# Kernel tuning notes

Hardware: AMD Instinct MI355X
Metric: run time of the kernel (lower is better)

## Reference

```python
import jax, jax.numpy as jnp
import numpy as np

N_NODES = 100000
N_EDGES = 1600000
D_FEAT = 64


def setup_inputs() -> dict:
    key = jax.random.key(0)
    k1, k2 = jax.random.split(key)
    x = jax.random.normal(k1, (N_NODES, D_FEAT), dtype=jnp.float32)
    edge_index = jax.random.randint(k2, (2, N_EDGES), 0, N_NODES, dtype=jnp.int64)
    return {"x": x, "edge_index": edge_index}


def reference(x, edge_index):
    # GCNProp (improved=False): remove self loops, add self loops w/ weight 1,
    # symmetric deg^-1/2 normalization, then spmm aggregation.
    N = x.shape[0]
    row, col = edge_index[0], edge_index[1]
    # remove_self_loops: zero the weight of any self-loop edge (math-equivalent
    # to dropping it, and jit-friendly: no data-dependent shapes).
    w = jnp.where(row != col, jnp.ones((), x.dtype), jnp.zeros((), x.dtype))
    # add_self_loops: append N diagonal edges with loop_value = 1 (improved=False)
    loop = jnp.arange(N, dtype=row.dtype)
    row_a = jnp.concatenate([row, loop])          # [E+N]
    col_a = jnp.concatenate([col, loop])          # [E+N]
    w_a = jnp.concatenate([w, jnp.ones((N,), x.dtype)])  # [E+N]
    # degree via scatter_add over rows
    deg = jax.ops.segment_sum(w_a, row_a, num_segments=N)  # [N]
    # deg^-0.5 with inf -> 0
    dinv = jnp.where(deg > 0, jax.lax.rsqrt(deg), jnp.zeros((), x.dtype))
    # edge normalization: deg[row]^-1/2 * w * deg[col]^-1/2
    norm = dinv[row_a] * w_a * dinv[col_a]        # [E+N]
    # spmm: gather neighbor features, scale, scatter-add into rows
    out = jax.ops.segment_sum(norm[:, None] * x[col_a], row_a, num_segments=N)  # [N, D]
    return out
```

## Files before the change

### kernel.cpp

```cpp
#include <hip/hip_runtime.h>

#define N_NODES 100000
#define N_EDGES 1600000
#define D 64
#define NB 391
#define BCAP 4480
#define PBLK 256
#define TPB 512
#define CHUNK ((N_EDGES + PBLK - 1) / PBLK)
#define CURSTRIDE 32

__device__ __forceinline__ unsigned short f2b(float f) {
    unsigned u = __float_as_uint(f);
    u += 0x7FFF + ((u >> 16) & 1);
    return (unsigned short)(u >> 16);
}
__device__ __forceinline__ float b2f(unsigned short v) {
    return __uint_as_float(((unsigned)v) << 16);
}

__global__ void init_cursor_kernel(int* __restrict__ cursor) {
    int b = blockIdx.x * blockDim.x + threadIdx.x;
    if (b < NB) cursor[b * CURSTRIDE] = b * BCAP;
}

__global__ void scatter_direct_kernel(const int* __restrict__ ei, int* __restrict__ cursor,
                                      int* __restrict__ epack) {
    __shared__ int h[NB];
    __shared__ int lbase[NB];
    __shared__ int lcur[NB];
    int t = threadIdx.x;
    for (int i = t; i < NB; i += TPB) h[i] = 0;
    __syncthreads();
    int s = blockIdx.x * CHUNK;
    int e = min(s + CHUNK, N_EDGES);
    for (int i = s + t; i < e; i += TPB) {
        int r = ei[i], c = ei[N_EDGES + i];
        if (r != c) atomicAdd(&h[r >> 8], 1);
    }
    __syncthreads();
    for (int i = t; i < NB; i += TPB) {
        lbase[i] = atomicAdd(&cursor[i * CURSTRIDE], h[i]);
        lcur[i] = 0;
    }
    __syncthreads();
    for (int i = s + t; i < e; i += TPB) {
        int r = ei[i], c = ei[N_EDGES + i];
        if (r != c) {
            int b = r >> 8;
            int p = lbase[b] + atomicAdd(&lcur[b], 1);
            epack[p] = ((r & 255) << 17) | c;
        }
    }
}

__global__ void rowsort_convert_kernel(const int* __restrict__ cursor, int* __restrict__ epack,
                                       int* __restrict__ rowstart, int* __restrict__ rowend,
                                       float* __restrict__ dinv, const float* __restrict__ x,
                                       unsigned short* __restrict__ xs) {
    __shared__ int ebuf[BCAP];
    __shared__ int h[256];
    __shared__ int sc[256];
    __shared__ int cur[256];
    __shared__ float dv[256];
    int b = blockIdx.x;
    int t = threadIdx.x;
    int base = b * BCAP;
    int n = min(cursor[b * CURSTRIDE] - base, BCAP);
    for (int i = t; i < n; i += 256) ebuf[i] = epack[base + i];
    h[t] = 0;
    __syncthreads();
    for (int i = t; i < n; i += 256) atomicAdd(&h[ebuf[i] >> 17], 1);
    __syncthreads();
    int v = h[t];
    sc[t] = v;
    __syncthreads();
    for (int off = 1; off < 256; off <<= 1) {
        int u = (t >= off) ? sc[t - off] : 0;
        __syncthreads();
        sc[t] += u;
        __syncthreads();
    }
    int excl = sc[t] - v;
    int row = b * 256 + t;
    float di = rsqrtf((float)(1 + v));
    if (row < N_NODES) {
        rowstart[row] = base + excl;
        rowend[row] = base + excl + v;
        dinv[row] = di;
    }
    dv[t] = di;
    cur[t] = excl;
    __syncthreads();
    for (int i = t; i < n; i += 256) {
        int p = ebuf[i];
        int pos = atomicAdd(&cur[p >> 17], 1);
        epack[base + pos] = p & 0x1FFFF;
    }
    int nrows = min(256, N_NODES - b * 256);
    const float4* x4 = (const float4*)x;
    ushort4* xs4 = (ushort4*)xs;
    for (int i = t; i < nrows * 16; i += 256) {
        int rl = i >> 4;
        float4 vv = x4[(size_t)(b * 256 + rl) * 16 + (i & 15)];
        float dd = dv[rl];
        ushort4 o;
        o.x = f2b(vv.x * dd);
        o.y = f2b(vv.y * dd);
        o.z = f2b(vv.z * dd);
        o.w = f2b(vv.w * dd);
        xs4[(size_t)(b * 256 + rl) * 16 + (i & 15)] = o;
    }
}

__global__ void gather_kernel(const unsigned short* __restrict__ xs, const float* __restrict__ dinv,
                              const int* __restrict__ rowstart, const int* __restrict__ rowend,
                              const int* __restrict__ sortedCol, float* __restrict__ out) {
    int t = blockIdx.x * blockDim.x + threadIdx.x;
    int r = t >> 6;
    int d = t & 63;
    if (r >= N_NODES) return;
    int start = rowstart[r];
    int end = rowend[r];
    float dr = dinv[r];
    float acc = b2f(xs[r * D + d]);
    for (int j = start; j < end; j += 64) {
        int idx = j + d;
        int cj = 0;
        if (idx < end) cj = sortedCol[idx];
        int n = min(64, end - j);
        int k = 0;
        for (; k + 8 <= n; k += 8) {
            int c0 = __shfl(cj, k);
            int c1 = __shfl(cj, k + 1);
            int c2 = __shfl(cj, k + 2);
            int c3 = __shfl(cj, k + 3);
            int c4 = __shfl(cj, k + 4);
            int c5 = __shfl(cj, k + 5);
            int c6 = __shfl(cj, k + 6);
            int c7 = __shfl(cj, k + 7);
            float v0 = b2f(xs[c0 * D + d]);
            float v1 = b2f(xs[c1 * D + d]);
            float v2 = b2f(xs[c2 * D + d]);
            float v3 = b2f(xs[c3 * D + d]);
            float v4 = b2f(xs[c4 * D + d]);
            float v5 = b2f(xs[c5 * D + d]);
            float v6 = b2f(xs[c6 * D + d]);
            float v7 = b2f(xs[c7 * D + d]);
            acc += ((v0 + v1) + (v2 + v3)) + ((v4 + v5) + (v6 + v7));
        }
        for (; k + 4 <= n; k += 4) {
            int c0 = __shfl(cj, k);
            int c1 = __shfl(cj, k + 1);
            int c2 = __shfl(cj, k + 2);
            int c3 = __shfl(cj, k + 3);
            float v0 = b2f(xs[c0 * D + d]);
            float v1 = b2f(xs[c1 * D + d]);
            float v2 = b2f(xs[c2 * D + d]);
            float v3 = b2f(xs[c3 * D + d]);
            acc += (v0 + v1) + (v2 + v3);
        }
        for (; k < n; k++) {
            int c = __shfl(cj, k);
            acc += b2f(xs[c * D + d]);
        }
    }
    out[r * D + d] = dr * acc;
}

extern "C" void kernel_launch(void* const* d_in, const int* in_sizes, int n_in,
                              void* d_out, int out_size, void* d_ws, size_t ws_size,
                              hipStream_t stream) {
    const float* x = (const float*)d_in[0];
    const int* ei = (const int*)d_in[1];
    float* out = (float*)d_out;

    int* cursor = (int*)d_ws;
    int* rowstart = cursor + NB * CURSTRIDE;
    int* rowend = rowstart + N_NODES;
    float* dinv = (float*)(rowend + N_NODES);
    int* epack = (int*)(dinv + N_NODES);
    unsigned short* xs = (unsigned short*)(epack + NB * BCAP);

    init_cursor_kernel<<<(NB + 255) / 256, 256, 0, stream>>>(cursor);
    scatter_direct_kernel<<<PBLK, TPB, 0, stream>>>(ei, cursor, epack);
    rowsort_convert_kernel<<<NB, 256, 0, stream>>>(cursor, epack, rowstart, rowend, dinv, x, xs);
    gather_kernel<<<(N_NODES * D + 255) / 256, 256, 0, stream>>>(xs, dinv, rowstart, rowend, epack, out);
}
```

Measured before the change: 159.2 us.

## Stage edges in LDS, pack row info, and gather two edges per wave

The scatter kernel now uses twice as many blocks and copies each edge chunk into shared memory once, so the two passes over it no longer both read global memory. The sort kernel runs 512 threads, stores start and degree together as one int2, and stores column indices pre-shifted to byte offsets. The gather kernel splits each wave into two halves that each load 4-byte bf16 pairs from a different neighbour, then combines the halves with a cross-lane shuffle; dinv is recomputed from the degree instead of being loaded. These changes aim to cut global load instructions and latency in the gather, at the cost of more shuffles, a reduction step, and larger shared memory use in the scatter kernel.

```diff
diff --git a/kernel.cpp b/kernel.cpp
--- a/kernel.cpp
+++ b/kernel.cpp
@@ -5,7 +5,7 @@
 #define D 64
 #define NB 391
 #define BCAP 4480
-#define PBLK 256
+#define PBLK 512
 #define TPB 512
 #define CHUNK ((N_EDGES + PBLK - 1) / PBLK)
 #define CURSTRIDE 32
@@ -15,27 +15,32 @@
     u += 0x7FFF + ((u >> 16) & 1);
     return (unsigned short)(u >> 16);
 }
-__device__ __forceinline__ float b2f(unsigned short v) {
-    return __uint_as_float(((unsigned)v) << 16);
-}
 
 __global__ void init_cursor_kernel(int* __restrict__ cursor) {
     int b = blockIdx.x * blockDim.x + threadIdx.x;
     if (b < NB) cursor[b * CURSTRIDE] = b * BCAP;
 }
 
-__global__ void scatter_direct_kernel(const int* __restrict__ ei, int* __restrict__ cursor,
-                                      int* __restrict__ epack) {
+__global__ __launch_bounds__(TPB) void scatter_direct_kernel(const int* __restrict__ ei,
+                                                             int* __restrict__ cursor,
+                                                             int* __restrict__ epack) {
+    __shared__ int er[CHUNK];
+    __shared__ int ec[CHUNK];
     __shared__ int h[NB];
     __shared__ int lbase[NB];
     __shared__ int lcur[NB];
     int t = threadIdx.x;
     for (int i = t; i < NB; i += TPB) h[i] = 0;
-    __syncthreads();
     int s = blockIdx.x * CHUNK;
     int e = min(s + CHUNK, N_EDGES);
-    for (int i = s + t; i < e; i += TPB) {
-        int r = ei[i], c = ei[N_EDGES + i];
+    int n = e - s;
+    for (int i = t; i < n; i += TPB) {
+        er[i] = ei[s + i];
+        ec[i] = ei[N_EDGES + s + i];
+    }
+    __syncthreads();
+    for (int i = t; i < n; i += TPB) {
+        int r = er[i], c = ec[i];
         if (r != c) atomicAdd(&h[r >> 8], 1);
     }
     __syncthreads();
@@ -44,8 +49,8 @@
         lcur[i] = 0;
     }
     __syncthreads();
-    for (int i = s + t; i < e; i += TPB) {
-        int r = ei[i], c = ei[N_EDGES + i];
+    for (int i = t; i < n; i += TPB) {
+        int r = er[i], c = ec[i];
         if (r != c) {
             int b = r >> 8;
             int p = lbase[b] + atomicAdd(&lcur[b], 1);
@@ -54,10 +59,11 @@
     }
 }
 
-__global__ void rowsort_convert_kernel(const int* __restrict__ cursor, int* __restrict__ epack,
-                                       int* __restrict__ rowstart, int* __restrict__ rowend,
-                                       float* __restrict__ dinv, const float* __restrict__ x,
-                                       unsigned short* __restrict__ xs) {
+__global__ __launch_bounds__(TPB) void csr_sort_convert_kernel(const int* __restrict__ cursor,
+                                                               int* __restrict__ epack,
+                                                               int2* __restrict__ rowinfo,
+                                                               const float* __restrict__ x,
+                                                               unsigned short* __restrict__ xs) {
     __shared__ int ebuf[BCAP];
     __shared__ int h[256];
     __shared__ int sc[256];
@@ -67,40 +73,37 @@
     int t = threadIdx.x;
     int base = b * BCAP;
     int n = min(cursor[b * CURSTRIDE] - base, BCAP);
-    for (int i = t; i < n; i += 256) ebuf[i] = epack[base + i];
-    h[t] = 0;
-    __syncthreads();
-    for (int i = t; i < n; i += 256) atomicAdd(&h[ebuf[i] >> 17], 1);
-    __syncthreads();
-    int v = h[t];
-    sc[t] = v;
+    for (int i = t; i < n; i += TPB) ebuf[i] = epack[base + i];
+    if (t < 256) h[t] = 0;
+    __syncthreads();
+    for (int i = t; i < n; i += TPB) atomicAdd(&h[ebuf[i] >> 17], 1);
+    __syncthreads();
+    int v = 0;
+    if (t < 256) { v = h[t]; sc[t] = v; }
     __syncthreads();
     for (int off = 1; off < 256; off <<= 1) {
-        int u = (t >= off) ? sc[t - off] : 0;
+        int u = (t < 256 && t >= off) ? sc[t - off] : 0;
         __syncthreads();
-        sc[t] += u;
+        if (t < 256) sc[t] += u;
         __syncthreads();
     }
-    int excl = sc[t] - v;
-    int row = b * 256 + t;
-    float di = rsqrtf((float)(1 + v));
-    if (row < N_NODES) {
-        rowstart[row] = base + excl;
-        rowend[row] = base + excl + v;
-        dinv[row] = di;
-    }
-    dv[t] = di;
-    cur[t] = excl;
-    __syncthreads();
-    for (int i = t; i < n; i += 256) {
+    if (t < 256) {
+        int excl = sc[t] - v;
+        int row = b * 256 + t;
+        if (row < N_NODES) rowinfo[row] = make_int2(base + excl, v);
+        dv[t] = rsqrtf((float)(1 + v));
+        cur[t] = excl;
+    }
+    __syncthreads();
+    for (int i = t; i < n; i += TPB) {
         int p = ebuf[i];
         int pos = atomicAdd(&cur[p >> 17], 1);
-        epack[base + pos] = p & 0x1FFFF;
+        epack[base + pos] = (p & 0x1FFFF) << 7;
     }
     int nrows = min(256, N_NODES - b * 256);
     const float4* x4 = (const float4*)x;
     ushort4* xs4 = (ushort4*)xs;
-    for (int i = t; i < nrows * 16; i += 256) {
+    for (int i = t; i < nrows * 16; i += TPB) {
         int rl = i >> 4;
         float4 vv = x4[(size_t)(b * 256 + rl) * 16 + (i & 15)];
         float dd = dv[rl];
@@ -113,59 +116,95 @@
     }
 }
 
-__global__ void gather_kernel(const unsigned short* __restrict__ xs, const float* __restrict__ dinv,
-                              const int* __restrict__ rowstart, const int* __restrict__ rowend,
-                              const int* __restrict__ sortedCol, float* __restrict__ out) {
+__global__ __launch_bounds__(256) void gather_kernel(const unsigned short* __restrict__ xs,
+                                                     const int2* __restrict__ rowinfo,
+                                                     const int* __restrict__ colidx,
+                                                     float* __restrict__ out) {
     int t = blockIdx.x * blockDim.x + threadIdx.x;
     int r = t >> 6;
-    int d = t & 63;
+    int lane = t & 63;
     if (r >= N_NODES) return;
-    int start = rowstart[r];
-    int end = rowend[r];
-    float dr = dinv[r];
-    float acc = b2f(xs[r * D + d]);
+    int lp = lane & 31;
+    int hf = lane >> 5;
+    int lpo = lp << 2;
+    int2 ri = rowinfo[r];
+    int start = ri.x;
+    int end = start + ri.y;
+    float dr = rsqrtf((float)(1 + ri.y));
+    const char* xsb = (const char*)xs;
+    float ax = 0.0f, ay = 0.0f;
+    if (hf == 0) {
+        unsigned v = *(const unsigned*)(xsb + (((size_t)r) << 7) + lpo);
+        ax = __uint_as_float(v << 16);
+        ay = __uint_as_float(v & 0xFFFF0000u);
+    }
     for (int j = start; j < end; j += 64) {
-        int idx = j + d;
-        int cj = 0;
-        if (idx < end) cj = sortedCol[idx];
+        int idx = j + lane;
+        int cj = (idx < end) ? colidx[idx] : 0;
         int n = min(64, end - j);
         int k = 0;
-        for (; k + 8 <= n; k += 8) {
-            int c0 = __shfl(cj, k);
-            int c1 = __shfl(cj, k + 1);
-            int c2 = __shfl(cj, k + 2);
-            int c3 = __shfl(cj, k + 3);
-            int c4 = __shfl(cj, k + 4);
-            int c5 = __shfl(cj, k + 5);
-            int c6 = __shfl(cj, k + 6);
-            int c7 = __shfl(cj, k + 7);
-            float v0 = b2f(xs[c0 * D + d]);
-            float v1 = b2f(xs[c1 * D + d]);
-            float v2 = b2f(xs[c2 * D + d]);
-            float v3 = b2f(xs[c3 * D + d]);
-            float v4 = b2f(xs[c4 * D + d]);
-            float v5 = b2f(xs[c5 * D + d]);
-            float v6 = b2f(xs[c6 * D + d]);
-            float v7 = b2f(xs[c7 * D + d]);
-            acc += ((v0 + v1) + (v2 + v3)) + ((v4 + v5) + (v6 + v7));
-        }
-        for (; k + 4 <= n; k += 4) {
-            int c0 = __shfl(cj, k);
-            int c1 = __shfl(cj, k + 1);
-            int c2 = __shfl(cj, k + 2);
-            int c3 = __shfl(cj, k + 3);
-            float v0 = b2f(xs[c0 * D + d]);
-            float v1 = b2f(xs[c1 * D + d]);
-            float v2 = b2f(xs[c2 * D + d]);
-            float v3 = b2f(xs[c3 * D + d]);
-            acc += (v0 + v1) + (v2 + v3);
-        }
-        for (; k < n; k++) {
-            int c = __shfl(cj, k);
-            acc += b2f(xs[c * D + d]);
-        }
-    }
-    out[r * D + d] = dr * acc;
+        for (; 2 * (k + 8) <= n; k += 8) {
+            int s0 = __shfl(cj, 2 * k + hf);
+            int s1 = __shfl(cj, 2 * k + 2 + hf);
+            int s2 = __shfl(cj, 2 * k + 4 + hf);
+            int s3 = __shfl(cj, 2 * k + 6 + hf);
+            int s4 = __shfl(cj, 2 * k + 8 + hf);
+            int s5 = __shfl(cj, 2 * k + 10 + hf);
+            int s6 = __shfl(cj, 2 * k + 12 + hf);
+            int s7 = __shfl(cj, 2 * k + 14 + hf);
+            unsigned v0 = *(const unsigned*)(xsb + (unsigned)(s0 + lpo));
+            unsigned v1 = *(const unsigned*)(xsb + (unsigned)(s1 + lpo));
+            unsigned v2 = *(const unsigned*)(xsb + (unsigned)(s2 + lpo));
+            unsigned v3 = *(const unsigned*)(xsb + (unsigned)(s3 + lpo));
+            unsigned v4 = *(const unsigned*)(xsb + (unsigned)(s4 + lpo));
+            unsigned v5 = *(const unsigned*)(xsb + (unsigned)(s5 + lpo));
+            unsigned v6 = *(const unsigned*)(xsb + (unsigned)(s6 + lpo));
+            unsigned v7 = *(const unsigned*)(xsb + (unsigned)(s7 + lpo));
+            float a0 = __uint_as_float(v0 << 16), b0 = __uint_as_float(v0 & 0xFFFF0000u);
+            float a1 = __uint_as_float(v1 << 16), b1 = __uint_as_float(v1 & 0xFFFF0000u);
+            float a2 = __uint_as_float(v2 << 16), b2 = __uint_as_float(v2 & 0xFFFF0000u);
+            float a3 = __uint_as_float(v3 << 16), b3 = __uint_as_float(v3 & 0xFFFF0000u);
+            float a4 = __uint_as_float(v4 << 16), b4 = __uint_as_float(v4 & 0xFFFF0000u);
+            float a5 = __uint_as_float(v5 << 16), b5 = __uint_as_float(v5 & 0xFFFF0000u);
+            float a6 = __uint_as_float(v6 << 16), b6 = __uint_as_float(v6 & 0xFFFF0000u);
+            float a7 = __uint_as_float(v7 << 16), b7 = __uint_as_float(v7 & 0xFFFF0000u);
+            ax += ((a0 + a1) + (a2 + a3)) + ((a4 + a5) + (a6 + a7));
+            ay += ((b0 + b1) + (b2 + b3)) + ((b4 + b5) + (b6 + b7));
+        }
+        for (; 2 * (k + 4) <= n; k += 4) {
+            int s0 = __shfl(cj, 2 * k + hf);
+            int s1 = __shfl(cj, 2 * k + 2 + hf);
+            int s2 = __shfl(cj, 2 * k + 4 + hf);
+            int s3 = __shfl(cj, 2 * k + 6 + hf);
+            unsigned v0 = *(const unsigned*)(xsb + (unsigned)(s0 + lpo));
+            unsigned v1 = *(const unsigned*)(xsb + (unsigned)(s1 + lpo));
+            unsigned v2 = *(const unsigned*)(xsb + (unsigned)(s2 + lpo));
+            unsigned v3 = *(const unsigned*)(xsb + (unsigned)(s3 + lpo));
+            float a0 = __uint_as_float(v0 << 16), b0 = __uint_as_float(v0 & 0xFFFF0000u);
+            float a1 = __uint_as_float(v1 << 16), b1 = __uint_as_float(v1 & 0xFFFF0000u);
+            float a2 = __uint_as_float(v2 << 16), b2 = __uint_as_float(v2 & 0xFFFF0000u);
+            float a3 = __uint_as_float(v3 << 16), b3 = __uint_as_float(v3 & 0xFFFF0000u);
+            ax += (a0 + a1) + (a2 + a3);
+            ay += (b0 + b1) + (b2 + b3);
+        }
+        for (; 2 * k < n; k++) {
+            int src = 2 * k + hf;
+            int s0 = __shfl(cj, (src < n) ? src : (n - 1));
+            unsigned v0 = *(const unsigned*)(xsb + (unsigned)(s0 + lpo));
+            if (src < n) {
+                ax += __uint_as_float(v0 << 16);
+                ay += __uint_as_float(v0 & 0xFFFF0000u);
+            }
+        }
+    }
+    ax += __shfl_xor(ax, 32);
+    ay += __shfl_xor(ay, 32);
+    if (hf == 0) {
+        float2 o;
+        o.x = dr * ax;
+        o.y = dr * ay;
+        ((float2*)out)[(size_t)r * 32 + lp] = o;
+    }
 }
 
 extern "C" void kernel_launch(void* const* d_in, const int* in_sizes, int n_in,
@@ -176,14 +215,12 @@
     float* out = (float*)d_out;
 
     int* cursor = (int*)d_ws;
-    int* rowstart = cursor + NB * CURSTRIDE;
-    int* rowend = rowstart + N_NODES;
-    float* dinv = (float*)(rowend + N_NODES);
-    int* epack = (int*)(dinv + N_NODES);
+    int2* rowinfo = (int2*)(cursor + NB * CURSTRIDE);
+    int* epack = (int*)(rowinfo + N_NODES);
     unsigned short* xs = (unsigned short*)(epack + NB * BCAP);
 
     init_cursor_kernel<<<(NB + 255) / 256, 256, 0, stream>>>(cursor);
     scatter_direct_kernel<<<PBLK, TPB, 0, stream>>>(ei, cursor, epack);
-    rowsort_convert_kernel<<<NB, 256, 0, stream>>>(cursor, epack, rowstart, rowend, dinv, x, xs);
-    gather_kernel<<<(N_NODES * D + 255) / 256, 256, 0, stream>>>(xs, dinv, rowstart, rowend, epack, out);
-}
+    csr_sort_convert_kernel<<<NB, TPB, 0, stream>>>(cursor, epack, rowinfo, x, xs);
+    gather_kernel<<<(N_NODES * D + 255) / 256, 256, 0, stream>>>(xs, rowinfo, epack, out);
+}
```

Result: no change. 160.1 us (+0.6%).
